# Optimization experiments

Measured on AMD Instinct MI355X. Metric: run time of the kernel, lower is better.

## Reference

```python
import jax, jax.numpy as jnp
import numpy as np

N_NODES = 50000
N_EDGES = 800000
IN_C, HID_C, OUT_C = 128, 128, 64


def setup_inputs() -> dict:
    key = jax.random.key(0)
    ks = jax.random.split(key, 8)
    sc_in = 1.0 / np.sqrt(IN_C)
    sc_hid = 1.0 / np.sqrt(HID_C)
    return {
        "x": jax.random.normal(ks[0], (N_NODES, IN_C), dtype=jnp.float32),
        "edge_index": jax.random.randint(ks[1], (2, N_EDGES), 0, N_NODES, dtype=jnp.int64),
        "W1_l": jax.random.normal(ks[2], (IN_C, HID_C), dtype=jnp.float32) * sc_in,
        "b1": jnp.zeros((HID_C,), dtype=jnp.float32),
        "W1_r": jax.random.normal(ks[3], (IN_C, HID_C), dtype=jnp.float32) * sc_in,
        "W2_l": jax.random.normal(ks[4], (HID_C, OUT_C), dtype=jnp.float32) * sc_hid,
        "b2": jnp.zeros((OUT_C,), dtype=jnp.float32),
        "W2_r": jax.random.normal(ks[5], (HID_C, OUT_C), dtype=jnp.float32) * sc_hid,
    }


def _sage_conv(x, src, dst, W_l, b, W_r, num_nodes):
    # gather neighbor features along edges: messages flow src -> dst
    msg = x[src]                                             # [E, C]
    agg = jax.ops.segment_sum(msg, dst, num_segments=num_nodes)
    cnt = jax.ops.segment_sum(jnp.ones((src.shape[0],), x.dtype), dst,
                              num_segments=num_nodes)
    mean = agg / jnp.maximum(cnt, 1.0)[:, None]              # mean aggregation
    # PyG SAGEConv: lin_l(aggregated) + lin_r(root); bias on lin_l only
    return mean @ W_l + b + x @ W_r


def reference(x, edge_index, W1_l, b1, W1_r, W2_l, b2, W2_r):
    src, dst = edge_index[0], edge_index[1]
    n = x.shape[0]
    h = jax.nn.relu(_sage_conv(x, src, dst, W1_l, b1, W1_r, n))
    # dropout(p=0.2) is identity at inference (training=False)
    return _sage_conv(h, src, dst, W2_l, b2, W2_r, n)
```

## Files before the change

kernel.cpp:

```cpp
#include <hip/hip_runtime.h>

#define N_NODES 50000
#define N_EDGES 800000
#define IN_C 128
#define HID_C 128
#define OUT_C 64

#define NBUCK 500
#define NODES_PER_BUCK 100
#define BCAP 2560
#define BA_CHUNK 8192
#define BA_BLOCKS ((N_EDGES + BA_CHUNK - 1) / BA_CHUNK)

#define XB_BLOCKS 6250
#define W1T_BLOCKS 128
#define W2T_BLOCKS 64
#define PREP_BLOCKS (XB_BLOCKS + W1T_BLOCKS + W2T_BLOCKS)
#define FUSED_BLOCKS (BA_BLOCKS + PREP_BLOCKS)

typedef __bf16 bf16x8 __attribute__((ext_vector_type(8)));
typedef __bf16 bf16x4 __attribute__((ext_vector_type(4)));
typedef float  f32x4  __attribute__((ext_vector_type(4)));

__global__ __launch_bounds__(256) void prep_bucketA_kernel(const float* __restrict__ x,
                                                           const float* __restrict__ W1l,
                                                           const float* __restrict__ W1r,
                                                           const float* __restrict__ W2l,
                                                           const float* __restrict__ W2r,
                                                           __bf16* __restrict__ xb,
                                                           __bf16* __restrict__ W1T,
                                                           __bf16* __restrict__ W2T,
                                                           const int* __restrict__ src,
                                                           const int* __restrict__ dst,
                                                           int* __restrict__ cursor,
                                                           unsigned* __restrict__ ebuf) {
    __shared__ int cnt[NBUCK];
    __shared__ int gbase[NBUCK];
    __shared__ int lcur[NBUCK];
    const int blk = blockIdx.x, t = threadIdx.x;
    if (blk < BA_BLOCKS) {
        for (int i = t; i < NBUCK; i += 256) cnt[i] = 0;
        __syncthreads();
        const int e0 = blk * BA_CHUNK;
        const int e1 = (e0 + BA_CHUNK < N_EDGES) ? e0 + BA_CHUNK : N_EDGES;
        for (int e = e0 + t; e < e1; e += 256)
            atomicAdd(&cnt[dst[e] / NODES_PER_BUCK], 1);
        __syncthreads();
        for (int i = t; i < NBUCK; i += 256) {
            gbase[i] = i * BCAP + atomicAdd(&cursor[i], cnt[i]);
            lcur[i] = 0;
        }
        __syncthreads();
        for (int e = e0 + t; e < e1; e += 256) {
            int d = dst[e];
            int b = d / NODES_PER_BUCK;
            int idx = gbase[b] + atomicAdd(&lcur[b], 1);
            if (idx < (b + 1) * BCAP)
                ebuf[idx] = (unsigned)src[e] | ((unsigned)(d - b * NODES_PER_BUCK) << 16);
        }
        return;
    }
    const int b = blk - BA_BLOCKS;
    if (b < XB_BLOCKS) {
        int i = b * 256 + t;
        float4 v = ((const float4*)x)[i];
        bf16x4 o = { (__bf16)v.x, (__bf16)v.y, (__bf16)v.z, (__bf16)v.w };
        ((bf16x4*)xb)[i] = o;
    } else if (b < XB_BLOCKS + W1T_BLOCKS) {
        int i = (b - XB_BLOCKS) * 256 + t;
        int n = i >> 8, kk = i & 255;
        float v = (kk < 128) ? W1l[kk * 128 + n] : W1r[(kk - 128) * 128 + n];
        W1T[i] = (__bf16)v;
    } else {
        int i = (b - XB_BLOCKS - W1T_BLOCKS) * 256 + t;
        int n = i >> 7, k = i & 127;
        float v = (n < 64) ? W2l[k * 64 + n] : W2r[k * 64 + (n - 64)];
        W2T[i] = (__bf16)v;
    }
}

__global__ __launch_bounds__(256) void bucketB_kernel(const unsigned* __restrict__ ebuf,
                                                      const int* __restrict__ cursor,
                                                      int* __restrict__ row_ptr,
                                                      int* __restrict__ srcs) {
    __shared__ int psum[256];
    __shared__ int deg[NODES_PER_BUCK];
    __shared__ int ofs[NODES_PER_BUCK + 1];
    const int b = blockIdx.x, t = threadIdx.x;
    int part = 0;
    for (int i = t; i < b; i += 256) {
        int c = cursor[i];
        if (c > BCAP) c = BCAP;
        part += c;
    }
    psum[t] = part;
    __syncthreads();
    for (int off = 128; off > 0; off >>= 1) {
        if (t < off) psum[t] += psum[t + off];
        __syncthreads();
    }
    const int rbase = psum[0];
    int m = cursor[b];
    if (m > BCAP) m = BCAP;
    const int node0 = b * NODES_PER_BUCK;
    const unsigned* eb = ebuf + (size_t)b * BCAP;

    for (int i = t; i < NODES_PER_BUCK; i += 256) deg[i] = 0;
    __syncthreads();
    for (int i = t; i < m; i += 256)
        atomicAdd(&deg[eb[i] >> 16], 1);
    __syncthreads();
    if (t == 0) {
        int s = 0;
        for (int i = 0; i < NODES_PER_BUCK; ++i) { ofs[i] = s; s += deg[i]; }
        ofs[NODES_PER_BUCK] = s;
    }
    __syncthreads();
    for (int i = t; i < NODES_PER_BUCK; i += 256) row_ptr[node0 + i] = rbase + ofs[i];
    if (b == 0 && t == 0) row_ptr[N_NODES] = N_EDGES;
    for (int i = t; i < NODES_PER_BUCK; i += 256) deg[i] = ofs[i];
    __syncthreads();
    for (int i = t; i < m; i += 256) {
        unsigned p = eb[i];
        int d = (int)(p >> 16);
        int pos = atomicAdd(&deg[d], 1);
        srcs[rbase + pos] = (int)(p & 0xFFFFu);
    }
}

__global__ __launch_bounds__(256) void agg_x_kernel(const __bf16* __restrict__ xb,
                                                    const int* __restrict__ row_ptr,
                                                    const int* __restrict__ srcs,
                                                    __bf16* __restrict__ m1) {
    const int wid = threadIdx.x >> 6, lane = threadIdx.x & 63;
    const int n = blockIdx.x * 4 + wid;
    if (n >= N_NODES) return;
    const int beg = row_ptr[n], end = row_ptr[n + 1];
    const int grp = lane >> 4;
    const int c   = lane & 15;
    float acc[8] = {};
    int s = beg + grp;
    for (; s + 12 < end; s += 16) {
        int u0 = srcs[s];
        int u1 = srcs[s + 4];
        int u2 = srcs[s + 8];
        int u3 = srcs[s + 12];
        bf16x8 v0 = *(const bf16x8*)(xb + (size_t)u0 * 128 + c * 8);
        bf16x8 v1 = *(const bf16x8*)(xb + (size_t)u1 * 128 + c * 8);
        bf16x8 v2 = *(const bf16x8*)(xb + (size_t)u2 * 128 + c * 8);
        bf16x8 v3 = *(const bf16x8*)(xb + (size_t)u3 * 128 + c * 8);
#pragma unroll
        for (int j = 0; j < 8; j++) acc[j] += (float)v0[j];
#pragma unroll
        for (int j = 0; j < 8; j++) acc[j] += (float)v1[j];
#pragma unroll
        for (int j = 0; j < 8; j++) acc[j] += (float)v2[j];
#pragma unroll
        for (int j = 0; j < 8; j++) acc[j] += (float)v3[j];
    }
    for (; s < end; s += 4) {
        int u = srcs[s];
        bf16x8 v = *(const bf16x8*)(xb + (size_t)u * 128 + c * 8);
#pragma unroll
        for (int j = 0; j < 8; j++) acc[j] += (float)v[j];
    }
#pragma unroll
    for (int j = 0; j < 8; j++) {
        acc[j] += __shfl_xor(acc[j], 16, 64);
        acc[j] += __shfl_xor(acc[j], 32, 64);
    }
    float cnt = (float)(end - beg);
    if (cnt < 1.f) cnt = 1.f;
    if (grp == 0) {
        bf16x8 o;
#pragma unroll
        for (int j = 0; j < 8; j++) o[j] = (__bf16)(acc[j] / cnt);
        *(bf16x8*)(m1 + (size_t)n * 128 + c * 8) = o;
    }
}

#define LDK 72
#define LDH 136

__global__ __launch_bounds__(256) void gemm12_kernel(const __bf16* __restrict__ A0,
                                                     const __bf16* __restrict__ A1,
                                                     const __bf16* __restrict__ W1T,
                                                     const __bf16* __restrict__ W2T,
                                                     const float* __restrict__ b1,
                                                     __bf16* __restrict__ Y,
                                                     float* __restrict__ Z, int M) {
    __shared__ __bf16 As[128 * LDH];
    __shared__ __bf16 Bs[128 * LDK];
    const int tid = threadIdx.x;
    const int row0 = blockIdx.x * 128;
    const int wave = tid >> 6, lane = tid & 63;
    const int wm = (wave & 1) * 64, wn = (wave >> 1) * 64;
    const int lr = lane & 15, quad = lane >> 4;

    f32x4 acc[4][4] = {};
    for (int ks = 0; ks < 256; ks += 64) {
        const __bf16* Asrc = (ks < 128) ? A0 : A1;
        const int kofs = (ks < 128) ? ks : ks - 128;
        for (int i = tid; i < 128 * 8; i += 256) {
            int r = i >> 3, ch = i & 7;
            int gr = row0 + r;
            float4 v = {0.f, 0.f, 0.f, 0.f};
            if (gr < M) v = *(const float4*)(Asrc + (size_t)gr * 128 + kofs + ch * 8);
            *(float4*)(As + r * LDH + ch * 8) = v;
        }
        for (int i = tid; i < 128 * 8; i += 256) {
            int r = i >> 3, ch = i & 7;
            float4 v = *(const float4*)(W1T + (size_t)r * 256 + ks + ch * 8);
            *(float4*)(Bs + r * LDK + ch * 8) = v;
        }
        __syncthreads();
#pragma unroll
        for (int k0 = 0; k0 < 64; k0 += 32) {
            bf16x8 af[4], bfr[4];
#pragma unroll
            for (int mt = 0; mt < 4; mt++)
                af[mt] = *(const bf16x8*)(As + (wm + mt * 16 + lr) * LDH + k0 + quad * 8);
#pragma unroll
            for (int nt = 0; nt < 4; nt++)
                bfr[nt] = *(const bf16x8*)(Bs + (wn + nt * 16 + lr) * LDK + k0 + quad * 8);
#pragma unroll
            for (int mt = 0; mt < 4; mt++)
#pragma unroll
                for (int nt = 0; nt < 4; nt++)
                    acc[mt][nt] = __builtin_amdgcn_mfma_f32_16x16x32_bf16(af[mt], bfr[nt], acc[mt][nt], 0, 0, 0);
        }
        __syncthreads();
    }

#pragma unroll
    for (int mt = 0; mt < 4; mt++) {
#pragma unroll
        for (int r = 0; r < 4; r++) {
            int row = wm + mt * 16 + quad * 4 + r;
#pragma unroll
            for (int nt = 0; nt < 4; nt++) {
                int col = wn + nt * 16 + lr;
                float v = acc[mt][nt][r] + b1[col];
                v = v > 0.f ? v : 0.f;
                As[row * LDH + col] = (__bf16)v;
            }
        }
    }

    f32x4 acc2[4][4] = {};
    for (int kh = 0; kh < 128; kh += 64) {
        for (int i = tid; i < 128 * 8; i += 256) {
            int r = i >> 3, ch = i & 7;
            float4 v = *(const float4*)(W2T + (size_t)r * 128 + kh + ch * 8);
            *(float4*)(Bs + r * LDK + ch * 8) = v;
        }
        __syncthreads();
#pragma unroll
        for (int k0 = 0; k0 < 64; k0 += 32) {
            bf16x8 af[4], bfr[4];
#pragma unroll
            for (int mt = 0; mt < 4; mt++)
                af[mt] = *(const bf16x8*)(As + (wm + mt * 16 + lr) * LDH + kh + k0 + quad * 8);
#pragma unroll
            for (int nt = 0; nt < 4; nt++)
                bfr[nt] = *(const bf16x8*)(Bs + (wn + nt * 16 + lr) * LDK + k0 + quad * 8);
#pragma unroll
            for (int mt = 0; mt < 4; mt++)
#pragma unroll
                for (int nt = 0; nt < 4; nt++)
                    acc2[mt][nt] = __builtin_amdgcn_mfma_f32_16x16x32_bf16(af[mt], bfr[nt], acc2[mt][nt], 0, 0, 0);
        }
        __syncthreads();
    }

#pragma unroll
    for (int mt = 0; mt < 4; mt++) {
#pragma unroll
        for (int r = 0; r < 4; r++) {
            int gr = row0 + wm + mt * 16 + quad * 4 + r;
            if (gr >= M) continue;
#pragma unroll
            for (int nt = 0; nt < 4; nt++) {
                int gc = wn + nt * 16 + lr;
                float v = acc2[mt][nt][r];
                if (gc < 64) Y[(size_t)gr * 64 + gc] = (__bf16)v;
                else         Z[(size_t)gr * 64 + (gc - 64)] = v;
            }
        }
    }
}

__global__ __launch_bounds__(256) void agg2_kernel(const __bf16* __restrict__ Y,
                                                   const float* __restrict__ Z,
                                                   const int* __restrict__ row_ptr,
                                                   const int* __restrict__ srcs,
                                                   const float* __restrict__ b2,
                                                   float* __restrict__ out) {
    const int wid = threadIdx.x >> 6, lane = threadIdx.x & 63;
    const int n = blockIdx.x * 4 + wid;
    if (n >= N_NODES) return;
    const int beg = row_ptr[n], end = row_ptr[n + 1];
    const int grp = lane >> 3;
    const int c   = lane & 7;
    float4 z0 = {0,0,0,0}, z1 = {0,0,0,0}, bb0 = {0,0,0,0}, bb1 = {0,0,0,0};
    if (grp == 0) {
        z0 = *(const float4*)(Z + (size_t)n * 64 + c * 8);
        z1 = *(const float4*)(Z + (size_t)n * 64 + c * 8 + 4);
        bb0 = *(const float4*)(b2 + c * 8);
        bb1 = *(const float4*)(b2 + c * 8 + 4);
    }
    float acc[8] = {};
    int s = beg + grp;
    for (; s + 8 < end; s += 16) {
        int u0 = srcs[s];
        int u1 = srcs[s + 8];
        bf16x8 v0 = *(const bf16x8*)(Y + (size_t)u0 * 64 + c * 8);
        bf16x8 v1 = *(const bf16x8*)(Y + (size_t)u1 * 64 + c * 8);
#pragma unroll
        for (int j = 0; j < 8; j++) acc[j] += (float)v0[j];
#pragma unroll
        for (int j = 0; j < 8; j++) acc[j] += (float)v1[j];
    }
    if (s < end) {
        int u = srcs[s];
        bf16x8 v = *(const bf16x8*)(Y + (size_t)u * 64 + c * 8);
#pragma unroll
        for (int j = 0; j < 8; j++) acc[j] += (float)v[j];
    }
#pragma unroll
    for (int j = 0; j < 8; j++) {
        acc[j] += __shfl_xor(acc[j], 8, 64);
        acc[j] += __shfl_xor(acc[j], 16, 64);
        acc[j] += __shfl_xor(acc[j], 32, 64);
    }
    float cnt = (float)(end - beg);
    if (cnt < 1.f) cnt = 1.f;
    if (grp == 0) {
        float inv = 1.f / cnt;
        float4 o0 = { acc[0] * inv + bb0.x + z0.x, acc[1] * inv + bb0.y + z0.y,
                      acc[2] * inv + bb0.z + z0.z, acc[3] * inv + bb0.w + z0.w };
        float4 o1 = { acc[4] * inv + bb1.x + z1.x, acc[5] * inv + bb1.y + z1.y,
                      acc[6] * inv + bb1.z + z1.z, acc[7] * inv + bb1.w + z1.w };
        *(float4*)(out + (size_t)n * 64 + c * 8) = o0;
        *(float4*)(out + (size_t)n * 64 + c * 8 + 4) = o1;
    }
}


extern "C" void kernel_launch(void* const* d_in, const int* in_sizes, int n_in,
                              void* d_out, int out_size, void* d_ws, size_t ws_size,
                              hipStream_t stream) {
    const float* x   = (const float*)d_in[0];
    const int*   ei  = (const int*)d_in[1];
    const float* W1l = (const float*)d_in[2];
    const float* b1  = (const float*)d_in[3];
    const float* W1r = (const float*)d_in[4];
    const float* W2l = (const float*)d_in[5];
    const float* b2  = (const float*)d_in[6];
    const float* W2r = (const float*)d_in[7];
    float* out = (float*)d_out;

    size_t need = 0;
    auto count = [&](size_t bytes) { need += (bytes + 255) & ~(size_t)255; };
    count((size_t)NBUCK * BCAP * 4);
    count((size_t)NBUCK * 4);
    count((size_t)(N_NODES + 1) * 4);
    count((size_t)N_EDGES * 4);
    count((size_t)N_NODES * 128 * 2);
    count((size_t)128 * 256 * 2);
    count((size_t)128 * 128 * 2);
    count((size_t)N_NODES * 128 * 2);
    count((size_t)N_NODES * 64 * 2);
    count((size_t)N_NODES * 64 * 4);
    if (ws_size < need) return;

    char* ws = (char*)d_ws;
    size_t off = 0;
    auto alloc = [&](size_t bytes) -> void* {
        void* p = ws + off;
        off += (bytes + 255) & ~(size_t)255;
        return p;
    };
    unsigned* ebuf  = (unsigned*)alloc((size_t)NBUCK * BCAP * 4);
    int*    cursor  = (int*)alloc((size_t)NBUCK * 4);
    int*    row_ptr = (int*)alloc((size_t)(N_NODES + 1) * 4);
    int*    srcs    = (int*)alloc((size_t)N_EDGES * 4);
    __bf16* xb      = (__bf16*)alloc((size_t)N_NODES * 128 * 2);
    __bf16* W1T     = (__bf16*)alloc((size_t)128 * 256 * 2);
    __bf16* W2T     = (__bf16*)alloc((size_t)128 * 128 * 2);
    __bf16* m1      = (__bf16*)alloc((size_t)N_NODES * 128 * 2);
    __bf16* Y       = (__bf16*)alloc((size_t)N_NODES * 64 * 2);
    float*  Z       = (float*)alloc((size_t)N_NODES * 64 * 4);

    const int* src = ei;
    const int* dst = ei + N_EDGES;

    hipMemsetAsync(cursor, 0, (size_t)NBUCK * 4, stream);
    prep_bucketA_kernel<<<FUSED_BLOCKS, 256, 0, stream>>>(x, W1l, W1r, W2l, W2r,
                                                          xb, W1T, W2T,
                                                          src, dst, cursor, ebuf);
    bucketB_kernel<<<NBUCK, 256, 0, stream>>>(ebuf, cursor, row_ptr, srcs);
    agg_x_kernel<<<(N_NODES + 3) / 4, 256, 0, stream>>>(xb, row_ptr, srcs, m1);
    gemm12_kernel<<<(N_NODES + 127) / 128, 256, 0, stream>>>(m1, xb, W1T, W2T, b1, Y, Z, N_NODES);
    agg2_kernel<<<(N_NODES + 3) / 4, 256, 0, stream>>>(Y, Z, row_ptr, srcs, b2, out);
}
```

Baseline: 198.8 us.

## Vectorize edge bucketing loads, pad global cursors, widen x conversion

Edge bucketing now reads dst and src as int4, handling four edges per thread, and uses a smaller chunk so there are twice as many bucketing blocks. The global per-bucket cursors are padded to one per 64 bytes to reduce atomic contention and false sharing. The x-to-bf16 conversion handles eight elements per thread with half as many blocks. The vectorized loops assume the edge count per chunk is a multiple of four, which holds for these sizes, and the memset grows slightly.

```diff
diff --git a/kernel.cpp b/kernel.cpp
--- a/kernel.cpp
+++ b/kernel.cpp
@@ -9,10 +9,11 @@
 #define NBUCK 500
 #define NODES_PER_BUCK 100
 #define BCAP 2560
-#define BA_CHUNK 8192
+#define CURS_STRIDE 16
+#define BA_CHUNK 4096
 #define BA_BLOCKS ((N_EDGES + BA_CHUNK - 1) / BA_CHUNK)
 
-#define XB_BLOCKS 6250
+#define XB_BLOCKS 3125
 #define W1T_BLOCKS 128
 #define W2T_BLOCKS 64
 #define PREP_BLOCKS (XB_BLOCKS + W1T_BLOCKS + W2T_BLOCKS)
@@ -43,29 +44,58 @@
         __syncthreads();
         const int e0 = blk * BA_CHUNK;
         const int e1 = (e0 + BA_CHUNK < N_EDGES) ? e0 + BA_CHUNK : N_EDGES;
-        for (int e = e0 + t; e < e1; e += 256)
-            atomicAdd(&cnt[dst[e] / NODES_PER_BUCK], 1);
+        const int nE = e1 - e0;
+        for (int q = 4 * t; q + 3 < nE; q += 1024) {
+            int4 d4 = *(const int4*)(dst + e0 + q);
+            atomicAdd(&cnt[d4.x / NODES_PER_BUCK], 1);
+            atomicAdd(&cnt[d4.y / NODES_PER_BUCK], 1);
+            atomicAdd(&cnt[d4.z / NODES_PER_BUCK], 1);
+            atomicAdd(&cnt[d4.w / NODES_PER_BUCK], 1);
+        }
         __syncthreads();
         for (int i = t; i < NBUCK; i += 256) {
-            gbase[i] = i * BCAP + atomicAdd(&cursor[i], cnt[i]);
+            gbase[i] = i * BCAP + atomicAdd(&cursor[i * CURS_STRIDE], cnt[i]);
             lcur[i] = 0;
         }
         __syncthreads();
-        for (int e = e0 + t; e < e1; e += 256) {
-            int d = dst[e];
-            int b = d / NODES_PER_BUCK;
-            int idx = gbase[b] + atomicAdd(&lcur[b], 1);
-            if (idx < (b + 1) * BCAP)
-                ebuf[idx] = (unsigned)src[e] | ((unsigned)(d - b * NODES_PER_BUCK) << 16);
+        for (int q = 4 * t; q + 3 < nE; q += 1024) {
+            int4 s4 = *(const int4*)(src + e0 + q);
+            int4 d4 = *(const int4*)(dst + e0 + q);
+            {
+                int d = d4.x, b = d / NODES_PER_BUCK;
+                int idx = gbase[b] + atomicAdd(&lcur[b], 1);
+                if (idx < (b + 1) * BCAP)
+                    ebuf[idx] = (unsigned)s4.x | ((unsigned)(d - b * NODES_PER_BUCK) << 16);
+            }
+            {
+                int d = d4.y, b = d / NODES_PER_BUCK;
+                int idx = gbase[b] + atomicAdd(&lcur[b], 1);
+                if (idx < (b + 1) * BCAP)
+                    ebuf[idx] = (unsigned)s4.y | ((unsigned)(d - b * NODES_PER_BUCK) << 16);
+            }
+            {
+                int d = d4.z, b = d / NODES_PER_BUCK;
+                int idx = gbase[b] + atomicAdd(&lcur[b], 1);
+                if (idx < (b + 1) * BCAP)
+                    ebuf[idx] = (unsigned)s4.z | ((unsigned)(d - b * NODES_PER_BUCK) << 16);
+            }
+            {
+                int d = d4.w, b = d / NODES_PER_BUCK;
+                int idx = gbase[b] + atomicAdd(&lcur[b], 1);
+                if (idx < (b + 1) * BCAP)
+                    ebuf[idx] = (unsigned)s4.w | ((unsigned)(d - b * NODES_PER_BUCK) << 16);
+            }
         }
         return;
     }
     const int b = blk - BA_BLOCKS;
     if (b < XB_BLOCKS) {
         int i = b * 256 + t;
-        float4 v = ((const float4*)x)[i];
-        bf16x4 o = { (__bf16)v.x, (__bf16)v.y, (__bf16)v.z, (__bf16)v.w };
-        ((bf16x4*)xb)[i] = o;
+        float4 v0 = ((const float4*)x)[2 * i];
+        float4 v1 = ((const float4*)x)[2 * i + 1];
+        bf16x8 o = { (__bf16)v0.x, (__bf16)v0.y, (__bf16)v0.z, (__bf16)v0.w,
+                     (__bf16)v1.x, (__bf16)v1.y, (__bf16)v1.z, (__bf16)v1.w };
+        ((bf16x8*)xb)[i] = o;
     } else if (b < XB_BLOCKS + W1T_BLOCKS) {
         int i = (b - XB_BLOCKS) * 256 + t;
         int n = i >> 8, kk = i & 255;
@@ -89,7 +119,7 @@
     const int b = blockIdx.x, t = threadIdx.x;
     int part = 0;
     for (int i = t; i < b; i += 256) {
-        int c = cursor[i];
+        int c = cursor[i * CURS_STRIDE];
         if (c > BCAP) c = BCAP;
         part += c;
     }
@@ -100,7 +130,7 @@
         __syncthreads();
     }
     const int rbase = psum[0];
-    int m = cursor[b];
+    int m = cursor[b * CURS_STRIDE];
     if (m > BCAP) m = BCAP;
     const int node0 = b * NODES_PER_BUCK;
     const unsigned* eb = ebuf + (size_t)b * BCAP;
@@ -363,7 +393,7 @@
     size_t need = 0;
     auto count = [&](size_t bytes) { need += (bytes + 255) & ~(size_t)255; };
     count((size_t)NBUCK * BCAP * 4);
-    count((size_t)NBUCK * 4);
+    count((size_t)NBUCK * CURS_STRIDE * 4);
     count((size_t)(N_NODES + 1) * 4);
     count((size_t)N_EDGES * 4);
     count((size_t)N_NODES * 128 * 2);
@@ -382,7 +412,7 @@
         return p;
     };
     unsigned* ebuf  = (unsigned*)alloc((size_t)NBUCK * BCAP * 4);
-    int*    cursor  = (int*)alloc((size_t)NBUCK * 4);
+    int*    cursor  = (int*)alloc((size_t)NBUCK * CURS_STRIDE * 4);
     int*    row_ptr = (int*)alloc((size_t)(N_NODES + 1) * 4);
     int*    srcs    = (int*)alloc((size_t)N_EDGES * 4);
     __bf16* xb      = (__bf16*)alloc((size_t)N_NODES * 128 * 2);
@@ -395,7 +425,7 @@
     const int* src = ei;
     const int* dst = ei + N_EDGES;
 
-    hipMemsetAsync(cursor, 0, (size_t)NBUCK * 4, stream);
+    hipMemsetAsync(cursor, 0, (size_t)NBUCK * CURS_STRIDE * 4, stream);
     prep_bucketA_kernel<<<FUSED_BLOCKS, 256, 0, stream>>>(x, W1l, W1r, W2l, W2r,
                                                           xb, W1T, W2T,
                                                           src, dst, cursor, ebuf);
```

Result: faster. 183.3 us (median of 2 runs) (-7.8%).
